# Kernel optimization log

Measured on AMD Instinct MI355X. Metric: run time of the kernel, lower is better.

## Reference

```python
import jax, jax.numpy as jnp
import numpy as np

OUTPUT_SIZE = (48, 48, 48)
TRUNCATION = (32, 32, 32)
HOMOMORPHIC = False


def dct_mat(N):
    """Orthonormal DCT-II matrix M so that y = M @ x matches scipy dct(x, norm='ortho')."""
    n = jnp.arange(N, dtype=jnp.float32)
    k = n[:, None]
    M = jnp.cos(jnp.pi * (n[None, :] + 0.5) * k / N) * jnp.sqrt(2.0 / N)
    M = M.at[0].mul(1.0 / jnp.sqrt(2.0))  # k=0 row scale -> sqrt(1/N)
    return M


def setup_inputs() -> dict:
    key = jax.random.key(0)
    x = jax.random.normal(key, (4, 32, 64, 64, 64), dtype=jnp.float32)
    return {"x": x}


def reference(x) -> jnp.ndarray:
    B, C, D, H, W = x.shape
    t0, t1, t2 = TRUNCATION
    o0, o1, o2 = OUTPUT_SIZE

    if HOMOMORPHIC:
        x = jnp.log(x + 1e-6)

    # 3D orthonormal DCT-II (separable, per axis)
    Md, Mh, Mw = dct_mat(D), dct_mat(H), dct_mat(W)
    xd = jnp.einsum('ad,bcdhw->bcahw', Md, x)
    xd = jnp.einsum('ah,bcdhw->bcdaw', Mh, xd)
    xd = jnp.einsum('aw,bcdhw->bcdha', Mw, xd)

    # crop low frequencies, zero-pad to output_size
    xc = xd[:, :, :t0, :t1, :t2]
    xp = jnp.pad(xc, ((0, 0), (0, 0), (0, o0 - t0), (0, o1 - t1), (0, o2 - t2)))

    # 3D orthonormal IDCT (DCT-III) = transpose of DCT-II matrix
    Id, Ih, Iw = dct_mat(o0).T, dct_mat(o1).T, dct_mat(o2).T
    y = jnp.einsum('ad,bcdhw->bcahw', Id, xp)
    y = jnp.einsum('ah,bcdhw->bcdaw', Ih, y)
    y = jnp.einsum('aw,bcdhw->bcdha', Iw, y)

    if HOMOMORPHIC:
        y = jnp.exp(y)
    return y
```

## Files before the change

kernel.cpp:

```cpp
#include <hip/hip_runtime.h>


typedef __attribute__((ext_vector_type(8))) short short8;
typedef __attribute__((ext_vector_type(4))) float f32x4;
typedef __attribute__((ext_vector_type(4))) unsigned int u32x4;
typedef __attribute__((ext_vector_type(2))) unsigned int u32x2;

static __device__ __forceinline__ unsigned short f2bf(float f) {
    unsigned int u = __float_as_uint(f);
    u += 0x7fffu + ((u >> 16) & 1u);
    return (unsigned short)(u >> 16);
}
static __device__ __forceinline__ float bf2f(unsigned short h) {
    return __uint_as_float(((unsigned int)h) << 16);
}

static __device__ __forceinline__ short8 ldtbl(const unsigned short* __restrict__ tbl,
                                               int s, int ks, int t, int l) {
    return *(const short8*)(tbl + (unsigned)((((s * 2 + ks) * 3 + t) * 64 + l) * 8));
}

__global__ __launch_bounds__(256) void gen_tbl(unsigned short* __restrict__ tbl) {
    int i = blockIdx.x * 256 + threadIdx.x;
    int j = i & 7;
    int lane = (i >> 3) & 63;
    int tks = i >> 9;
    int t = tks % 3, ks = tks / 3;
    int k = 8 * (lane >> 4) + j + 32 * ks;
    int a = 16 * t + (lane & 15);
    const float PI = 3.14159265358979323846f;
    const float s48 = 0.20412414523193150818f;
    const float s64 = 0.17677669529663688110f;
    float s = 0.f;
    for (int kk = 0; kk < 32; ++kk) {
        int m48 = ((2 * a + 1) * kk) % 192;
        int m64 = ((2 * k + 1) * kk) % 256;
        float c48 = cosf(PI * (float)m48 / 96.0f) * s48;
        float c64 = cosf(PI * (float)m64 / 128.0f) * s64;
        if (kk == 0) { c48 *= 0.70710678118654752440f; c64 *= 0.70710678118654752440f; }
        s += c48 * c64;
    }
    unsigned short hi = f2bf(s);
    unsigned short lo = f2bf(s - bf2f(hi));
    tbl[i] = hi;
    tbl[i + 3072] = lo;
}

#define SC_S 72
__global__ __launch_bounds__(256) void k1_wh(const float* __restrict__ x,
                                             const unsigned short* __restrict__ tbl,
                                             unsigned short* __restrict__ y2) {
    __shared__ unsigned short sC[48 * SC_S];

    const int tid = threadIdx.x;
    const int blk = blockIdx.x;
    const int g = __builtin_amdgcn_readfirstlane(tid >> 6);
    const int l = tid & 63;
    const int r = l & 15;
    const int kq = l >> 4;

    f32x4 z = {0.f, 0.f, 0.f, 0.f};
    f32x4 acc0 = z, acc1 = z, acc2 = z;
    const float* xb = x + (unsigned)(blk * 4096 + (16 * g + r) * 64 + kq * 8);
    #pragma unroll
    for (int ks = 0; ks < 2; ++ks) {
        float4 xa = *(const float4*)(xb + 32 * ks);
        float4 xc = *(const float4*)(xb + 32 * ks + 4);
        float v[8] = {xa.x, xa.y, xa.z, xa.w, xc.x, xc.y, xc.z, xc.w};
        short8 xh, xl;
        #pragma unroll
        for (int j = 0; j < 8; ++j) {
            unsigned int u = __float_as_uint(v[j]);
            float rem = v[j] - __uint_as_float(u & 0xffff0000u);
            xh[j] = (short)(u >> 16);
            xl[j] = (short)(__float_as_uint(rem) >> 16);
        }
        #pragma unroll
        for (int t = 0; t < 3; ++t) {
            short8 wh = ldtbl(tbl, 0, ks, t, l);
            f32x4 a = (t == 0) ? acc0 : (t == 1) ? acc1 : acc2;
            a = __builtin_amdgcn_mfma_f32_16x16x32_bf16(xh, wh, a, 0, 0, 0);
            a = __builtin_amdgcn_mfma_f32_16x16x32_bf16(xl, wh, a, 0, 0, 0);
            if (t == 0) acc0 = a; else if (t == 1) acc1 = a; else acc2 = a;
        }
    }
    #pragma unroll
    for (int t = 0; t < 3; ++t) {
        f32x4 a = (t == 0) ? acc0 : (t == 1) ? acc1 : acc2;
        u32x2 pk;
        pk[0] = (unsigned int)f2bf(a[0]) | ((unsigned int)f2bf(a[1]) << 16);
        pk[1] = (unsigned int)f2bf(a[2]) | ((unsigned int)f2bf(a[3]) << 16);
        *(u32x2*)&sC[(16 * t + r) * SC_S + 16 * g + 4 * kq] = pk;
    }
    __syncthreads();

    auto loadA = [&](int m, int ks) -> short8 {
        return *(const short8*)&sC[(16 * m + r) * SC_S + 8 * kq + 32 * ks];
    };
    auto storeY = [&](int m, int n, f32x4 c) {
        u32x2 pk;
        pk[0] = (unsigned int)f2bf(c[0]) | ((unsigned int)f2bf(c[1]) << 16);
        pk[1] = (unsigned int)f2bf(c[2]) | ((unsigned int)f2bf(c[3]) << 16);
        *(u32x2*)(y2 + (unsigned)(blk * 2304 + (16 * n + r) * 48 + 16 * m + 4 * kq)) = pk;
    };

    if (g < 3) {
        f32x4 c0 = z, c1 = z;
        #pragma unroll
        for (int ks = 0; ks < 2; ++ks) {
            short8 ah = ldtbl(tbl, 0, ks, g, l);
            c0 = __builtin_amdgcn_mfma_f32_16x16x32_bf16(loadA(0, ks), ah, c0, 0, 0, 0);
            c1 = __builtin_amdgcn_mfma_f32_16x16x32_bf16(loadA(1, ks), ah, c1, 0, 0, 0);
        }
        storeY(0, g, c0);
        storeY(1, g, c1);
    } else {
        f32x4 t0 = z, t1 = z, t2 = z;
        #pragma unroll
        for (int ks = 0; ks < 2; ++ks) {
            short8 ca = loadA(2, ks);
            t0 = __builtin_amdgcn_mfma_f32_16x16x32_bf16(ca, ldtbl(tbl, 0, ks, 0, l), t0, 0, 0, 0);
            t1 = __builtin_amdgcn_mfma_f32_16x16x32_bf16(ca, ldtbl(tbl, 0, ks, 1, l), t1, 0, 0, 0);
            t2 = __builtin_amdgcn_mfma_f32_16x16x32_bf16(ca, ldtbl(tbl, 0, ks, 2, l), t2, 0, 0, 0);
        }
        storeY(2, 0, t0);
        storeY(2, 1, t1);
        storeY(2, 2, t2);
    }
}

__global__ __launch_bounds__(256) void k2_d(const unsigned short* __restrict__ y2,
                                            const unsigned short* __restrict__ tbl,
                                            float* __restrict__ out) {
    __shared__ unsigned short sY[4 * 3 * 64 * 16];

    const int tid = threadIdx.x;
    const int blk = blockIdx.x;
    const int bc = blk / 12;
    const int quad = blk % 12;

    const unsigned short* yb = y2 + (unsigned)(bc * 64 * 2304 + quad * 4 * 48);
    #pragma unroll
    for (int jj = 0; jj < 6; ++jj) {
        int f = tid + 256 * jj;
        int d = f / 24;
        int p = f % 24;
        int a1l = p / 6;
        int q = p % 6;
        int a2 = q * 8;
        int m = a2 >> 4;
        int c0 = a2 & 15;
        u32x4 v = *(const u32x4*)(yb + (unsigned)(d * 2304 + a1l * 48 + a2));
        *(u32x4*)&sY[(((a1l * 3 + m) * 64) + d) * 16 + c0] = v;
    }
    __syncthreads();

    const int g = __builtin_amdgcn_readfirstlane(tid >> 6);
    const int l = tid & 63;
    const int r = l & 15;
    const int kq = l >> 4;
    const int a1 = quad * 4 + g;

    short8 th[2][3], tl[2][3];
    #pragma unroll
    for (int ks = 0; ks < 2; ++ks)
        #pragma unroll
        for (int n = 0; n < 3; ++n) {
            th[ks][n] = ldtbl(tbl, 0, ks, n, l);
            tl[ks][n] = ldtbl(tbl, 1, ks, n, l);
        }

    f32x4 z = {0.f, 0.f, 0.f, 0.f};
    f32x4 acc[3][3];
    #pragma unroll
    for (int m = 0; m < 3; ++m)
        #pragma unroll
        for (int n = 0; n < 3; ++n) acc[m][n] = z;

    #pragma unroll
    for (int m = 0; m < 3; ++m) {
        #pragma unroll
        for (int ks = 0; ks < 2; ++ks) {
            short8 ya;
            #pragma unroll
            for (int j = 0; j < 8; ++j)
                ya[j] = (short)sY[((g * 3 + m) * 64 + 8 * kq + 32 * ks + j) * 16 + r];
            #pragma unroll
            for (int n = 0; n < 3; ++n) {
                acc[m][n] = __builtin_amdgcn_mfma_f32_16x16x32_bf16(ya, th[ks][n], acc[m][n], 0, 0, 0);
                acc[m][n] = __builtin_amdgcn_mfma_f32_16x16x32_bf16(ya, tl[ks][n], acc[m][n], 0, 0, 0);
            }
        }
    }

    #pragma unroll
    for (int m = 0; m < 3; ++m)
        #pragma unroll
        for (int n = 0; n < 3; ++n) {
            float4 v;
            v.x = acc[m][n][0]; v.y = acc[m][n][1]; v.z = acc[m][n][2]; v.w = acc[m][n][3];
            float* dst = out + ((size_t)(bc * 48 + 16 * n + r) * 48 + a1) * 48 + 16 * m + 4 * kq;
            *(float4*)dst = v;
        }
}

extern "C" void kernel_launch(void* const* d_in, const int* in_sizes, int n_in,
                              void* d_out, int out_size, void* d_ws, size_t ws_size,
                              hipStream_t stream) {
    const float* x = (const float*)d_in[0];
    float* out = (float*)d_out;

    unsigned short* tbl = (unsigned short*)d_ws;
    unsigned short* y2 = (unsigned short*)((char*)d_ws + 65536);

    gen_tbl<<<12, 256, 0, stream>>>(tbl);
    k1_wh<<<128 * 64, 256, 0, stream>>>(x, tbl, y2);
    k2_d<<<128 * 12, 256, 0, stream>>>(y2, tbl, out);
}
```

Measured before the change: 61.59 us.

## Bake DCT tables at compile time, drop lo-part MFMAs, swizzle k2 LDS layout

Moves the combined DCT/IDCT coefficient table from a runtime generation kernel to a constexpr device array, removing one kernel launch. In k2_d, drops the low-order bf16 correction MFMAs, halving matrix-core work, and reorganises the shared-memory staging into a d-contiguous, XOR-swizzled layout. The A operand can then be read with one 16-byte LDS load instead of eight scalar 2-byte reads. Dropping the lo table reduces precision of the third-axis transform, which risks accuracy tolerance.

```diff
diff --git a/kernel.cpp b/kernel.cpp
--- a/kernel.cpp
+++ b/kernel.cpp
@@ -2,53 +2,94 @@
 
 
 typedef __attribute__((ext_vector_type(8))) short short8;
+typedef __attribute__((ext_vector_type(8))) unsigned short u16x8;
 typedef __attribute__((ext_vector_type(4))) float f32x4;
 typedef __attribute__((ext_vector_type(4))) unsigned int u32x4;
 typedef __attribute__((ext_vector_type(2))) unsigned int u32x2;
+
+constexpr double CPI   = 3.14159265358979323846264338327950288;
+constexpr double CS48  = 0.20412414523193150818310700622549;
+constexpr double CS64  = 0.17677669529663688110021109052621;
+constexpr double CISQ2 = 0.70710678118654752440084436210485;
+
+constexpr double ccos_raw(double x) {
+    double x2 = x * x, term = 1.0, s = 1.0;
+    for (int n = 1; n <= 13; ++n) { term *= -x2 / double((2 * n - 1) * (2 * n)); s += term; }
+    return s;
+}
+constexpr double ccos(double x) {
+    if (x > CPI) x = 2.0 * CPI - x;
+    double sgn = 1.0;
+    if (x > CPI * 0.5) { x = CPI - x; sgn = -1.0; }
+    return sgn * ccos_raw(x);
+}
+constexpr unsigned short f2bf_c(float f) {
+    if (f == 0.0f) return 0;
+    int sign = 0; double x = f;
+    if (x < 0) { sign = 1; x = -x; }
+    int e = 0;
+    while (x >= 2.0) { x *= 0.5; ++e; }
+    while (x < 1.0)  { x *= 2.0; --e; }
+    double v = x * 128.0;
+    long iv = (long)v; double fr = v - (double)iv;
+    long m = iv;
+    if (fr > 0.5 || (fr == 0.5 && (iv & 1))) ++m;
+    if (m == 256) { m = 128; ++e; }
+    return (unsigned short)((sign << 15) | ((e + 127) << 7) | (int)(m - 128));
+}
+
+struct CosTab48 { double v[192];
+    constexpr CosTab48() : v{} { for (int m = 0; m < 192; ++m) v[m] = ccos(CPI * m / 96.0) * CS48; } };
+struct CosTab64 { double v[256];
+    constexpr CosTab64() : v{} { for (int m = 0; m < 256; ++m) v[m] = ccos(CPI * m / 128.0) * CS64; } };
+constexpr CosTab48 CT48{};
+constexpr CosTab64 CT64{};
+
+struct Part512 { unsigned short hi[512];
+    constexpr Part512(int p) : hi{} {
+        int ks = p / 3, t = p % 3;
+        for (int i = 0; i < 512; ++i) {
+            int j = i & 7, l = i >> 3;
+            int k = 8 * (l >> 4) + j + 32 * ks;
+            int a = 16 * t + (l & 15);
+            double s = 0.0;
+            for (int kk = 0; kk < 32; ++kk) {
+                int m48 = ((2 * a + 1) * kk) % 192;
+                int m64 = ((2 * k + 1) * kk) % 256;
+                double c48 = CT48.v[m48], c64 = CT64.v[m64];
+                if (kk == 0) { c48 *= CISQ2; c64 *= CISQ2; }
+                s += c48 * c64;
+            }
+            hi[i] = f2bf_c((float)s);
+        }
+    }
+};
+constexpr Part512 TP0(0), TP1(1), TP2(2), TP3(3), TP4(4), TP5(5);
+
+struct AllTbl { alignas(16) unsigned short v[6][512];
+    constexpr AllTbl() : v{} {
+        for (int i = 0; i < 512; ++i) v[0][i] = TP0.hi[i];
+        for (int i = 0; i < 512; ++i) v[1][i] = TP1.hi[i];
+        for (int i = 0; i < 512; ++i) v[2][i] = TP2.hi[i];
+        for (int i = 0; i < 512; ++i) v[3][i] = TP3.hi[i];
+        for (int i = 0; i < 512; ++i) v[4][i] = TP4.hi[i];
+        for (int i = 0; i < 512; ++i) v[5][i] = TP5.hi[i];
+    }
+};
+__device__ constexpr AllTbl g_tbl{};
+
+static __device__ __forceinline__ short8 ldtbl(int ks, int t, int l) {
+    return *(const short8*)&g_tbl.v[ks * 3 + t][l * 8];
+}
 
 static __device__ __forceinline__ unsigned short f2bf(float f) {
     unsigned int u = __float_as_uint(f);
     u += 0x7fffu + ((u >> 16) & 1u);
     return (unsigned short)(u >> 16);
 }
-static __device__ __forceinline__ float bf2f(unsigned short h) {
-    return __uint_as_float(((unsigned int)h) << 16);
-}
-
-static __device__ __forceinline__ short8 ldtbl(const unsigned short* __restrict__ tbl,
-                                               int s, int ks, int t, int l) {
-    return *(const short8*)(tbl + (unsigned)((((s * 2 + ks) * 3 + t) * 64 + l) * 8));
-}
-
-__global__ __launch_bounds__(256) void gen_tbl(unsigned short* __restrict__ tbl) {
-    int i = blockIdx.x * 256 + threadIdx.x;
-    int j = i & 7;
-    int lane = (i >> 3) & 63;
-    int tks = i >> 9;
-    int t = tks % 3, ks = tks / 3;
-    int k = 8 * (lane >> 4) + j + 32 * ks;
-    int a = 16 * t + (lane & 15);
-    const float PI = 3.14159265358979323846f;
-    const float s48 = 0.20412414523193150818f;
-    const float s64 = 0.17677669529663688110f;
-    float s = 0.f;
-    for (int kk = 0; kk < 32; ++kk) {
-        int m48 = ((2 * a + 1) * kk) % 192;
-        int m64 = ((2 * k + 1) * kk) % 256;
-        float c48 = cosf(PI * (float)m48 / 96.0f) * s48;
-        float c64 = cosf(PI * (float)m64 / 128.0f) * s64;
-        if (kk == 0) { c48 *= 0.70710678118654752440f; c64 *= 0.70710678118654752440f; }
-        s += c48 * c64;
-    }
-    unsigned short hi = f2bf(s);
-    unsigned short lo = f2bf(s - bf2f(hi));
-    tbl[i] = hi;
-    tbl[i + 3072] = lo;
-}
 
 #define SC_S 72
 __global__ __launch_bounds__(256) void k1_wh(const float* __restrict__ x,
-                                             const unsigned short* __restrict__ tbl,
                                              unsigned short* __restrict__ y2) {
     __shared__ unsigned short sC[48 * SC_S];
 
@@ -77,7 +118,7 @@
         }
         #pragma unroll
         for (int t = 0; t < 3; ++t) {
-            short8 wh = ldtbl(tbl, 0, ks, t, l);
+            short8 wh = ldtbl(ks, t, l);
             f32x4 a = (t == 0) ? acc0 : (t == 1) ? acc1 : acc2;
             a = __builtin_amdgcn_mfma_f32_16x16x32_bf16(xh, wh, a, 0, 0, 0);
             a = __builtin_amdgcn_mfma_f32_16x16x32_bf16(xl, wh, a, 0, 0, 0);
@@ -108,7 +149,7 @@
         f32x4 c0 = z, c1 = z;
         #pragma unroll
         for (int ks = 0; ks < 2; ++ks) {
-            short8 ah = ldtbl(tbl, 0, ks, g, l);
+            short8 ah = ldtbl(ks, g, l);
             c0 = __builtin_amdgcn_mfma_f32_16x16x32_bf16(loadA(0, ks), ah, c0, 0, 0, 0);
             c1 = __builtin_amdgcn_mfma_f32_16x16x32_bf16(loadA(1, ks), ah, c1, 0, 0, 0);
         }
@@ -119,9 +160,9 @@
         #pragma unroll
         for (int ks = 0; ks < 2; ++ks) {
             short8 ca = loadA(2, ks);
-            t0 = __builtin_amdgcn_mfma_f32_16x16x32_bf16(ca, ldtbl(tbl, 0, ks, 0, l), t0, 0, 0, 0);
-            t1 = __builtin_amdgcn_mfma_f32_16x16x32_bf16(ca, ldtbl(tbl, 0, ks, 1, l), t1, 0, 0, 0);
-            t2 = __builtin_amdgcn_mfma_f32_16x16x32_bf16(ca, ldtbl(tbl, 0, ks, 2, l), t2, 0, 0, 0);
+            t0 = __builtin_amdgcn_mfma_f32_16x16x32_bf16(ca, ldtbl(ks, 0, l), t0, 0, 0, 0);
+            t1 = __builtin_amdgcn_mfma_f32_16x16x32_bf16(ca, ldtbl(ks, 1, l), t1, 0, 0, 0);
+            t2 = __builtin_amdgcn_mfma_f32_16x16x32_bf16(ca, ldtbl(ks, 2, l), t2, 0, 0, 0);
         }
         storeY(2, 0, t0);
         storeY(2, 1, t1);
@@ -130,28 +171,29 @@
 }
 
 __global__ __launch_bounds__(256) void k2_d(const unsigned short* __restrict__ y2,
-                                            const unsigned short* __restrict__ tbl,
                                             float* __restrict__ out) {
-    __shared__ unsigned short sY[4 * 3 * 64 * 16];
+    __shared__ unsigned short sY[4 * 3 * 16 * 64];
 
     const int tid = threadIdx.x;
     const int blk = blockIdx.x;
     const int bc = blk / 12;
     const int quad = blk % 12;
 
-    const unsigned short* yb = y2 + (unsigned)(bc * 64 * 2304 + quad * 4 * 48);
-    #pragma unroll
-    for (int jj = 0; jj < 6; ++jj) {
-        int f = tid + 256 * jj;
-        int d = f / 24;
-        int p = f % 24;
-        int a1l = p / 6;
-        int q = p % 6;
-        int a2 = q * 8;
-        int m = a2 >> 4;
-        int c0 = a2 & 15;
-        u32x4 v = *(const u32x4*)(yb + (unsigned)(d * 2304 + a1l * 48 + a2));
-        *(u32x4*)&sY[(((a1l * 3 + m) * 64) + d) * 16 + c0] = v;
+    const unsigned short* yb = y2 + (unsigned)(bc * 147456 + quad * 4 * 48);
+    unsigned int* S32 = (unsigned int*)sY;
+    const int dh = tid & 31;
+    #pragma unroll
+    for (int jj = 0; jj < 3; ++jj) {
+        int cp = (tid >> 5) + 8 * jj;
+        int a1l = cp & 3, q = cp >> 2;
+        int m = q >> 1, c0 = 8 * (q & 1);
+        u16x8 v0 = *(const u16x8*)(yb + (unsigned)((2 * dh) * 2304 + a1l * 48 + q * 8));
+        u16x8 v1 = *(const u16x8*)(yb + (unsigned)((2 * dh + 1) * 2304 + a1l * 48 + q * 8));
+        unsigned int base = (unsigned)(((a1l * 3 + m) * 16 + c0) * 32);
+        #pragma unroll
+        for (int e = 0; e < 8; ++e)
+            S32[base + e * 32 + (dh ^ (e << 2))] =
+                (unsigned int)v0[e] | ((unsigned int)v1[e] << 16);
     }
     __syncthreads();
 
@@ -161,14 +203,11 @@
     const int kq = l >> 4;
     const int a1 = quad * 4 + g;
 
-    short8 th[2][3], tl[2][3];
+    short8 th[2][3];
     #pragma unroll
     for (int ks = 0; ks < 2; ++ks)
         #pragma unroll
-        for (int n = 0; n < 3; ++n) {
-            th[ks][n] = ldtbl(tbl, 0, ks, n, l);
-            tl[ks][n] = ldtbl(tbl, 1, ks, n, l);
-        }
+        for (int n = 0; n < 3; ++n) th[ks][n] = ldtbl(ks, n, l);
 
     f32x4 z = {0.f, 0.f, 0.f, 0.f};
     f32x4 acc[3][3];
@@ -181,15 +220,11 @@
     for (int m = 0; m < 3; ++m) {
         #pragma unroll
         for (int ks = 0; ks < 2; ++ks) {
-            short8 ya;
+            short8 ya = *(const short8*)&sY[(unsigned)(((g * 3 + m) * 16 + r) * 64
+                                            + ((8 * kq + 32 * ks) ^ ((r & 7) << 3)))];
             #pragma unroll
-            for (int j = 0; j < 8; ++j)
-                ya[j] = (short)sY[((g * 3 + m) * 64 + 8 * kq + 32 * ks + j) * 16 + r];
-            #pragma unroll
-            for (int n = 0; n < 3; ++n) {
+            for (int n = 0; n < 3; ++n)
                 acc[m][n] = __builtin_amdgcn_mfma_f32_16x16x32_bf16(ya, th[ks][n], acc[m][n], 0, 0, 0);
-                acc[m][n] = __builtin_amdgcn_mfma_f32_16x16x32_bf16(ya, tl[ks][n], acc[m][n], 0, 0, 0);
-            }
         }
     }
 
@@ -210,10 +245,8 @@
     const float* x = (const float*)d_in[0];
     float* out = (float*)d_out;
 
-    unsigned short* tbl = (unsigned short*)d_ws;
-    unsigned short* y2 = (unsigned short*)((char*)d_ws + 65536);
-
-    gen_tbl<<<12, 256, 0, stream>>>(tbl);
-    k1_wh<<<128 * 64, 256, 0, stream>>>(x, tbl, y2);
-    k2_d<<<128 * 12, 256, 0, stream>>>(y2, tbl, out);
-}
+    unsigned short* y2 = (unsigned short*)d_ws;
+
+    k1_wh<<<128 * 64, 256, 0, stream>>>(x, y2);
+    k2_d<<<128 * 12, 256, 0, stream>>>(y2, out);
+}
```

Result: faster. 52.74 us (median of 2 runs) (-14.4%).
